# Kernel tuning notes

Hardware: AMD Instinct MI355X
Metric: run time of the kernel (lower is better)

The kernel has to match this reference:

```python
import jax, jax.numpy as jnp
import numpy as np

B, T, C, H = 4, 2048, 1024, 8
D = C // H


def _rope_tables(t, d, base=10000.0):
    inv = 1.0 / (base ** (jnp.arange(0, d, 2, dtype=jnp.float32) / d))
    freqs = jnp.outer(jnp.arange(t, dtype=jnp.float32), inv)  # (T, D/2)
    cos = jnp.concatenate([jnp.cos(freqs)] * 2, axis=-1)  # (T, D)
    sin = jnp.concatenate([jnp.sin(freqs)] * 2, axis=-1)
    return cos, sin


def _apply_rope(x, cos, sin):
    # x: (B,H,T,D); rotate-half RoPE
    d2 = x.shape[-1] // 2
    x1, x2 = x[..., :d2], x[..., d2:]
    rot = jnp.concatenate([-x2, x1], axis=-1)
    return x * cos + rot * sin


def setup_inputs() -> dict:
    key = jax.random.key(0)
    ks = jax.random.split(key, 8)
    x = jax.random.normal(ks[0], (B, T, C), jnp.float32)
    w = lambda k: jax.random.normal(k, (C, C), jnp.float32) * 0.02
    # trigram directions: 8 sign patterns in {-1,+1}^3, L2-normalized (as in get_trigrams + F.normalize)
    signs = np.array([[(1 if (i >> b) & 1 else -1) for b in range(3)] for i in range(8)], np.float32)
    head_dirs = jnp.asarray(signs / np.sqrt(3.0))
    return {
        'x': x,
        'Wq': w(ks[1]), 'Wk': w(ks[2]), 'Wv': w(ks[3]), 'Wo': w(ks[4]),
        'ln_g': jnp.ones((C,), jnp.float32), 'ln_b': jnp.zeros((C,), jnp.float32),
        'head_scales': jax.random.normal(ks[5], (H,), jnp.float32) * 0.1,
        'head_dirs': head_dirs,
    }


def reference(x, Wq, Wk, Wv, Wo, ln_g, ln_b, head_scales, head_dirs):
    b, t, c = x.shape
    h = head_dirs.shape[0]
    d = c // h
    scale = 1.0 / jnp.sqrt(jnp.asarray(d, x.dtype))
    # pre-LN
    mu = jnp.mean(x, axis=-1, keepdims=True)
    var = jnp.mean((x - mu) ** 2, axis=-1, keepdims=True)
    xn = (x - mu) * jax.lax.rsqrt(var + 1e-5) * ln_g + ln_b
    q = (xn @ Wq.T).reshape(b, t, h, d).transpose(0, 2, 1, 3)  # (B,H,T,D)
    k = (xn @ Wk.T).reshape(b, t, h, d).transpose(0, 2, 1, 3)
    v = (xn @ Wv.T).reshape(b, t, h, d).transpose(0, 2, 1, 3)
    cos, sin = _rope_tables(t, d)
    q = _apply_rope(q, cos, sin)
    k = _apply_rope(k, cos, sin)
    causal = jnp.tril(jnp.ones((t, t), bool))
    # standard causal SDPA
    scores = jnp.einsum('bhqd,bhkd->bhqk', q, k) * scale
    scores = jnp.where(causal, scores, -jnp.inf)
    attn = jax.nn.softmax(scores, axis=-1)
    out = jnp.einsum('bhqk,bhkd->bhqd', attn, v)
    # trigram geometric bias attention (rank-1 logits from first 3 dims)
    qp = jnp.einsum('bhtd,hd->bht', q[..., :3], head_dirs)
    kp = jnp.einsum('bhtd,hd->bht', k[..., :3], head_dirs)
    geo = qp[..., :, None] * kp[..., None, :]  # (B,H,T,T)
    geo = jnp.where(causal, geo, -jnp.inf)
    geo_attn = jax.nn.softmax(geo, axis=-1)
    geo_out = jnp.einsum('bhqk,bhkd->bhqd', geo_attn, v)
    out = out + head_scales[None, :, None, None] * jax.lax.stop_gradient(geo_out - out)
    out = out.transpose(0, 2, 1, 3).reshape(b, t, c) @ Wo.T
    return x + out
```

## Files before the change

### kernel.cpp

```cpp
#include <hip/hip_runtime.h>
#include <hip/hip_bf16.h>
#include <stdint.h>

#define BB 4
#define TT 2048
#define CC 1024
#define HH 8
#define DD 128

typedef unsigned short u16;
typedef unsigned int u32;
typedef unsigned long long u64;
typedef __attribute__((ext_vector_type(4))) float f32x4;
typedef __attribute__((ext_vector_type(16))) float f32x16;
typedef __attribute__((ext_vector_type(8))) __bf16 bf16x8;

__device__ __forceinline__ float bf2f(u16 u){ u32 x=((u32)u)<<16; float f; __builtin_memcpy(&f,&x,4); return f; }
__device__ __forceinline__ u16 f2bf(float f){ u32 x; __builtin_memcpy(&x,&f,4); x += 0x7fffu + ((x>>16)&1u); return (u16)(x>>16); }

__device__ __forceinline__ void gload16(const void* g, void* l){
  __builtin_amdgcn_global_load_lds((const __attribute__((address_space(1))) u32*)g,
                                   (__attribute__((address_space(3))) u32*)l, 16, 0, 0);
}
__device__ __forceinline__ f32x4 mfma16(bf16x8 a, bf16x8 b, f32x4 c){
  return __builtin_amdgcn_mfma_f32_16x16x32_bf16(a,b,c,0,0,0);
}
__device__ __forceinline__ f32x16 mfma32(bf16x8 a, bf16x8 b, f32x16 c){
  return __builtin_amdgcn_mfma_f32_32x32x16_bf16(a,b,c,0,0,0);
}
__device__ __forceinline__ u32 cvtpk(float lo, float hi){
  u32 r; asm("v_cvt_pk_bf16_f32 %0, %1, %2" : "=v"(r) : "v"(lo), "v"(hi)); return r;
}
__device__ __forceinline__ void pl32swap(u32& d, u32& s){
  asm volatile("v_permlane32_swap_b32 %0, %1" : "+v"(d), "+v"(s));
}
union FRAG { u32 u[4]; bf16x8 v; };

__global__ void ln_k(const float* __restrict__ x, const float* __restrict__ g,
                     const float* __restrict__ bta, u16* __restrict__ xn){
  int row = blockIdx.x, tid = threadIdx.x;
  const float4 v = ((const float4*)(x + (size_t)row*CC))[tid];
  float s = v.x+v.y+v.z+v.w;
  float ss = v.x*v.x+v.y*v.y+v.z*v.z+v.w*v.w;
  #pragma unroll
  for(int m=1;m<64;m<<=1){ s += __shfl_xor(s,m); ss += __shfl_xor(ss,m); }
  __shared__ float red[8];
  if((tid&63)==0){ red[tid>>6]=s; red[4+(tid>>6)]=ss; }
  __syncthreads();
  float ts = red[0]+red[1]+red[2]+red[3];
  float tss = red[4]+red[5]+red[6]+red[7];
  float mu = ts*(1.0f/CC);
  float rs = rsqrtf(tss*(1.0f/CC) - mu*mu + 1e-5f);
  int c0 = tid*4;
  ushort4 o;
  o.x = f2bf((v.x-mu)*rs*g[c0+0]+bta[c0+0]);
  o.y = f2bf((v.y-mu)*rs*g[c0+1]+bta[c0+1]);
  o.z = f2bf((v.z-mu)*rs*g[c0+2]+bta[c0+2]);
  o.w = f2bf((v.w-mu)*rs*g[c0+3]+bta[c0+3]);
  ((ushort4*)(xn + (size_t)row*CC))[tid] = o;
}

__global__ void wconv_k(const float* __restrict__ wq, const float* __restrict__ wk,
                        const float* __restrict__ wv, const float* __restrict__ wo,
                        u16* __restrict__ out){
  int i = blockIdx.x*256 + threadIdx.x;
  int sel = i>>18;
  const float* src = sel==0?wq: sel==1?wk: sel==2?wv:wo;
  float4 v = ((const float4*)src)[i & 262143];
  ushort4 o; o.x=f2bf(v.x); o.y=f2bf(v.y); o.z=f2bf(v.z); o.w=f2bf(v.w);
  ((ushort4*)out)[i] = o;
}

__global__ void rope_tab_k(float* __restrict__ cosT, float* __restrict__ sinT){
  int i = blockIdx.x*256 + threadIdx.x;
  int t = i>>6, j = i&63;
  float inv = powf(10000.0f, -(float)(2*j)*(1.0f/128.0f));
  float a = (float)t * inv;
  cosT[i] = cosf(a);
  sinT[i] = sinf(a);
}

__global__ void qpkp_k(const u16* __restrict__ Qb, const u16* __restrict__ Kb,
                       const float* __restrict__ dirs, const float* __restrict__ cosT,
                       const float* __restrict__ sinT, float* __restrict__ qp, float* __restrict__ kp){
  int idx = blockIdx.x*256 + threadIdx.x;
  int b = idx>>14, rem = idx & 16383;
  int h = rem>>11, t = rem & 2047;
  size_t base = ((size_t)(b*TT + t))*CC + h*DD;
  float qv = 0.f, kv = 0.f;
  #pragma unroll
  for(int d=0; d<3; d++){
    float c = cosT[t*64+d], s = sinT[t*64+d];
    float dr = dirs[h*3+d];
    qv += (bf2f(Qb[base+d])*c - bf2f(Qb[base+d+64])*s) * dr;
    kv += (bf2f(Kb[base+d])*c - bf2f(Kb[base+d+64])*s) * dr;
  }
  qp[idx] = qv; kp[idx] = kv;
}

__global__ void ropepack_k(u16* __restrict__ Qb, const u16* __restrict__ Kb,
                           u16* __restrict__ KF,
                           const float* __restrict__ cosT, const float* __restrict__ sinT){
  const float SL2 = 0.08838834764831845f * 1.442695040888963f;
  int bt = blockIdx.x, tid = threadIdx.x;
  int b = bt>>11, t = bt & (TT-1);
  int ks = t>>5, k31 = t&31;
  int p0 = tid*4;
  int h = p0>>6, d0 = p0&63;
  size_t i1 = (size_t)bt*CC + h*DD + d0;
  ushort4 q1v = *(const ushort4*)(Qb + i1);
  ushort4 q2v = *(const ushort4*)(Qb + i1 + 64);
  ushort4 k1v = *(const ushort4*)(Kb + i1);
  ushort4 k2v = *(const ushort4*)(Kb + i1 + 64);
  float4 cv = *(const float4*)(cosT + t*64 + d0);
  float4 sv = *(const float4*)(sinT + t*64 + d0);
  float q1[4] = {bf2f(q1v.x),bf2f(q1v.y),bf2f(q1v.z),bf2f(q1v.w)};
  float q2[4] = {bf2f(q2v.x),bf2f(q2v.y),bf2f(q2v.z),bf2f(q2v.w)};
  float k1[4] = {bf2f(k1v.x),bf2f(k1v.y),bf2f(k1v.z),bf2f(k1v.w)};
  float k2[4] = {bf2f(k2v.x),bf2f(k2v.y),bf2f(k2v.z),bf2f(k2v.w)};
  float cc[4] = {cv.x,cv.y,cv.z,cv.w};
  float ssn[4] = {sv.x,sv.y,sv.z,sv.w};
  ushort4 oq1, oq2, ok1, ok2;
  u16* oq1p = (u16*)&oq1; u16* oq2p = (u16*)&oq2;
  u16* ok1p = (u16*)&ok1; u16* ok2p = (u16*)&ok2;
  #pragma unroll
  for(int j=0;j<4;j++){
    oq1p[j] = f2bf((q1[j]*cc[j] - q2[j]*ssn[j])*SL2);
    oq2p[j] = f2bf((q2[j]*cc[j] + q1[j]*ssn[j])*SL2);
    ok1p[j] = f2bf(k1[j]*cc[j] - k2[j]*ssn[j]);
    ok2p[j] = f2bf(k2[j]*cc[j] + k1[j]*ssn[j]);
  }
  *(ushort4*)(Qb + i1)      = oq1;
  *(ushort4*)(Qb + i1 + 64) = oq2;
  int bh = b*HH + h;
  int d2 = d0 + 64;
  size_t o1 = (((size_t)(bh*64 + ks)*8) + (d0>>4))*512 + (((d0>>3)&1)*32 + k31)*8 + (d0&7);
  size_t o2 = (((size_t)(bh*64 + ks)*8) + (d2>>4))*512 + (((d2>>3)&1)*32 + k31)*8 + (d2&7);
  *(ushort4*)(KF + o1) = ok1;
  *(ushort4*)(KF + o2) = ok2;
}

template<int MODE>
__global__ __launch_bounds__(256) void gemm_k(const u16* __restrict__ A, const u16* __restrict__ W,
                                              u16* __restrict__ outb, float* __restrict__ outf,
                                              const float* __restrict__ resid){
  __shared__ __align__(16) u16 As[128*64];
  __shared__ __align__(16) u16 Bs[128*64];
  const int K = CC;
  int m0 = blockIdx.x*128, n0 = blockIdx.y*128;
  int tid = threadIdx.x, w = tid>>6, l = tid&63;
  int li = l&15, lg = l>>4;
  int wm = w>>1, wn = w&1;
  f32x4 acc[4][4] = {};
  for(int k0=0; k0<K; k0+=64){
    #pragma unroll
    for(int i=0;i<4;i++){
      int L = (w*4+i)*1024 + l*16;
      int row = L>>7;
      int colb = (L&127) ^ ((row&7)<<4);
      gload16(A + ((size_t)(m0+row)*K + k0 + (colb>>1)), (char*)As + (w*4+i)*1024);
      gload16(W + ((size_t)(n0+row)*K + k0 + (colb>>1)), (char*)Bs + (w*4+i)*1024);
    }
    __syncthreads();
    #pragma unroll
    for(int kc=0;kc<2;kc++){
      bf16x8 af[4], bfr[4];
      #pragma unroll
      for(int mi=0;mi<4;mi++){
        int row = wm*64 + mi*16 + li;
        int colb = (kc*64 + lg*16) ^ ((row&7)<<4);
        af[mi] = *(const bf16x8*)((const char*)As + row*128 + colb);
      }
      #pragma unroll
      for(int ni=0;ni<4;ni++){
        int row = wn*64 + ni*16 + li;
        int colb = (kc*64 + lg*16) ^ ((row&7)<<4);
        bfr[ni] = *(const bf16x8*)((const char*)Bs + row*128 + colb);
      }
      #pragma unroll
      for(int mi=0;mi<4;mi++){
        #pragma unroll
        for(int ni=0;ni<4;ni++)
          acc[mi][ni] = mfma16(af[mi], bfr[ni], acc[mi][ni]);
      }
    }
    __syncthreads();
  }
  #pragma unroll
  for(int mi=0;mi<4;mi++){
    #pragma unroll
    for(int ni=0;ni<4;ni++){
      if(MODE==4){
        int row0 = m0 + wm*64 + mi*16 + lg*4;
        int col = n0 + wn*64 + ni*16 + li;
        int t = row0 & 2047, b = row0>>11;
        int h = col>>7, d = col&127;
        int bh = b*HH + h;
        size_t o = (((size_t)(bh*64 + (t>>5))*8) + (d>>5)*2 + ((t>>4)&1))*512
                   + (((t>>3)&1)*32 + (d&31))*8 + (t&7);
        ushort4 pk;
        pk.x = f2bf(acc[mi][ni][0]); pk.y = f2bf(acc[mi][ni][1]);
        pk.z = f2bf(acc[mi][ni][2]); pk.w = f2bf(acc[mi][ni][3]);
        *(ushort4*)(outb + o) = pk;
      } else {
        #pragma unroll
        for(int r=0;r<4;r++){
          int row = m0 + wm*64 + mi*16 + lg*4 + r;
          int col = n0 + wn*64 + ni*16 + li;
          float v = acc[mi][ni][r];
          if(MODE==0){
            outb[(size_t)row*CC + col] = f2bf(v);
          } else {
            size_t o = (size_t)row*CC + col;
            outf[o] = v + resid[o];
          }
        }
      }
    }
  }
}

struct SegState { float m1, l1, m2, l2; f32x16 a1[4]; f32x16 a2[4]; };

__device__ __forceinline__ void run_seg(int t, int klo, int khi, int bh, int b, int h,
                                        int l5, int q31,
                                        const u16* __restrict__ Q, const u16* __restrict__ KF,
                                        const u16* __restrict__ VF, const float* __restrict__ qp,
                                        const float* __restrict__ kp, SegState& S){
  const f32x16 zf = {};
  S.m1 = -__builtin_inff(); S.l1 = 0.f; S.m2 = -__builtin_inff(); S.l2 = 0.f;
  #pragma unroll
  for(int dt=0;dt<4;dt++){ S.a1[dt] = zf; S.a2[dt] = zf; }
  if(khi <= klo) return;

  int q0 = t*32, q = q0 + q31;
  bf16x8 qf[8];
  {
    const u16* qbase = Q + ((size_t)(b*TT + q)*CC + h*DD);
    #pragma unroll
    for(int db=0;db<8;db++) qf[db] = *(const bf16x8*)(qbase + db*16 + l5*8);
  }
  const float L2E = 1.442695040888963f;
  bf16x8 qpf;
  {
    float qs = qp[(size_t)bh*TT + q] * L2E;
    u16 qh = f2bf(qs); float qhf = bf2f(qh);
    u16 ql = f2bf(qs - qhf);
    FRAG fq; fq.u[0] = l5? 0u : ((u32)qh | ((u32)qh<<16));
    fq.u[1] = l5? 0u : (u32)ql; fq.u[2]=0; fq.u[3]=0;
    qpf = fq.v;
  }
  const u16* kfp = KF + (size_t)bh*64*4096 + (size_t)klo*4096 + (size_t)(q31 + 32*l5)*8;
  const u16* vfp = VF + (size_t)bh*64*4096 + (size_t)klo*4096 + (size_t)(q31 + 32*l5)*8;
  const float* kpp = kp + (size_t)bh*TT + q31;

  for(int is=klo; is<khi; ++is){
    int ksub = is*32;

    bf16x8 kf0 = *(const bf16x8*)(kfp + 0*512);
    bf16x8 kf1 = *(const bf16x8*)(kfp + 1*512);
    bf16x8 kf2 = *(const bf16x8*)(kfp + 2*512);
    bf16x8 kf3 = *(const bf16x8*)(kfp + 3*512);
    bf16x8 kf4 = *(const bf16x8*)(kfp + 4*512);
    bf16x8 kf5 = *(const bf16x8*)(kfp + 5*512);
    bf16x8 kf6 = *(const bf16x8*)(kfp + 6*512);
    bf16x8 kf7 = *(const bf16x8*)(kfp + 7*512);

    f32x16 s0 = {}, s1a = {};
    __builtin_amdgcn_s_setprio(1);
    s0  = mfma32(kf0, qf[0], s0);  s1a = mfma32(kf1, qf[1], s1a);
    s0  = mfma32(kf2, qf[2], s0);  s1a = mfma32(kf3, qf[3], s1a);
    s0  = mfma32(kf4, qf[4], s0);  s1a = mfma32(kf5, qf[5], s1a);
    s0  = mfma32(kf6, qf[6], s0);  s1a = mfma32(kf7, qf[7], s1a);
    __builtin_amdgcn_s_setprio(0);

    f32x16 gg;
    {
      const f32x16 zf2 = {};
      float kpv = kpp[ksub];
      u16 kh = f2bf(kpv); float khf = bf2f(kh);
      u16 kl = f2bf(kpv - khf);
      FRAG fk; fk.u[0] = l5? 0u : ((u32)kh | ((u32)kl<<16));
      fk.u[1] = l5? 0u : (u32)kh; fk.u[2]=0; fk.u[3]=0;
      gg = mfma32(fk.v, qpf, zf2);
    }

    float sv[16], gv[16];
    #pragma unroll
    for(int rr=0;rr<16;rr++){ sv[rr] = s0[rr]+s1a[rr]; gv[rr] = gg[rr]; }
    if(ksub + 31 > q0){
      #pragma unroll
      for(int rr=0;rr<16;rr++){
        int kg = ksub + (rr&3) + 8*(rr>>2) + 4*l5;
        if(kg > q){ sv[rr] = -__builtin_inff(); gv[rr] = -__builtin_inff(); }
      }
    }

    float mx=-__builtin_inff(), gx=-__builtin_inff();
    #pragma unroll
    for(int rr=0;rr<16;rr++){ mx = fmaxf(mx, sv[rr]); gx = fmaxf(gx, gv[rr]); }
    mx = fmaxf(mx, __shfl_xor(mx,32));
    gx = fmaxf(gx, __shfl_xor(gx,32));
    if(__ballot((mx > S.m1+8.f) | (gx > S.m2+8.f))){
      float mn1 = fmaxf(S.m1,mx), mn2 = fmaxf(S.m2,gx);
      float c1 = exp2f(S.m1-mn1), c2 = exp2f(S.m2-mn2);
      S.l1 *= c1; S.l2 *= c2; S.m1 = mn1; S.m2 = mn2;
      #pragma unroll
      for(int dt=0;dt<4;dt++){ S.a1[dt] *= c1; S.a2[dt] *= c2; }
    }
    float rs1=0.f, rs2=0.f;
    float e1[16], e2[16];
    #pragma unroll
    for(int rr=0;rr<16;rr++){
      e1[rr] = exp2f(sv[rr] - S.m1); rs1 += e1[rr];
      e2[rr] = exp2f(gv[rr] - S.m2); rs2 += e2[rr];
    }
    rs1 += __shfl_xor(rs1,32); rs2 += __shfl_xor(rs2,32);
    S.l1 += rs1; S.l2 += rs2;

    u32 P1[8], P2[8];
    #pragma unroll
    for(int m=0;m<8;m++){ P1[m] = cvtpk(e1[2*m], e1[2*m+1]); P2[m] = cvtpk(e2[2*m], e2[2*m+1]); }
    pl32swap(P1[0],P1[2]); pl32swap(P1[1],P1[3]); pl32swap(P1[4],P1[6]); pl32swap(P1[5],P1[7]);
    pl32swap(P2[0],P2[2]); pl32swap(P2[1],P2[3]); pl32swap(P2[4],P2[6]); pl32swap(P2[5],P2[7]);

    #pragma unroll
    for(int kb2=0;kb2<2;kb2++){
      FRAG f1, f2;
      #pragma unroll
      for(int j2=0;j2<4;j2++){ f1.u[j2] = P1[kb2*4+j2]; f2.u[j2] = P2[kb2*4+j2]; }
      bf16x8 pb1 = f1.v, pb2 = f2.v;
      bf16x8 vf0 = *(const bf16x8*)(vfp + (0+kb2)*512);
      bf16x8 vf1 = *(const bf16x8*)(vfp + (2+kb2)*512);
      bf16x8 vf2 = *(const bf16x8*)(vfp + (4+kb2)*512);
      bf16x8 vf3 = *(const bf16x8*)(vfp + (6+kb2)*512);
      __builtin_amdgcn_s_setprio(1);
      S.a1[0] = mfma32(vf0, pb1, S.a1[0]);  S.a2[0] = mfma32(vf0, pb2, S.a2[0]);
      S.a1[1] = mfma32(vf1, pb1, S.a1[1]);  S.a2[1] = mfma32(vf1, pb2, S.a2[1]);
      S.a1[2] = mfma32(vf2, pb1, S.a1[2]);  S.a2[2] = mfma32(vf2, pb2, S.a2[2]);
      S.a1[3] = mfma32(vf3, pb1, S.a1[3]);  S.a2[3] = mfma32(vf3, pb2, S.a2[3]);
      __builtin_amdgcn_s_setprio(0);
    }
    kfp += 4096; vfp += 4096;
  }
}

__global__ __launch_bounds__(128,2) void attn_k(const u16* __restrict__ Q, const u16* __restrict__ KF,
                                                const u16* __restrict__ VF, const float* __restrict__ qp,
                                                const float* __restrict__ kp, const float* __restrict__ hs,
                                                u16* __restrict__ outp){
  __shared__ __align__(16) float lp1[4*64*16];
  __shared__ __align__(16) float lp2[4*64*16];
  __shared__ float lml[32*4];
  int bid = blockIdx.x;
  int xcd = bid&7, r = bid>>3;
  int bh = xcd*4 + (r&3);
  int p = r>>2;
  int b = bh>>3, h = bh&7;
  int tid = threadIdx.x, w = tid>>6, l = tid&63;
  int l5 = l>>5, q31 = l&31;
  float sh = hs[h];

  SegState S;
  if(w==0){
    run_seg(p, 0, p+1, bh, b, h, l5, q31, Q, KF, VF, qp, kp, S);
    {
      float rl1 = 1.0f/S.l1, rl2 = 1.0f/S.l2;
      int q = p*32 + q31;
      u16* obase = outp + (size_t)(b*TT + q)*CC + h*DD;
      #pragma unroll
      for(int dt=0;dt<4;dt++){
        #pragma unroll
        for(int m=0;m<8;m++){
          float oa1 = S.a1[dt][2*m]*rl1,   oa2 = S.a2[dt][2*m]*rl2;
          float ob1 = S.a1[dt][2*m+1]*rl1, ob2 = S.a2[dt][2*m+1]*rl2;
          float oa = oa1 + sh*(oa2-oa1);
          float ob = ob1 + sh*(ob2-ob1);
          int d = dt*32 + (2*m&3) + 8*(m>>1) + 4*l5;
          *(u32*)(obase + d) = cvtpk(oa, ob);
        }
      }
    }
    run_seg(63-p, 0, 31-p, bh, b, h, l5, q31, Q, KF, VF, qp, kp, S);
    #pragma unroll
    for(int dt=0;dt<4;dt++){
      *(f32x16*)&lp1[(dt*64 + l)*16] = S.a1[dt];
      *(f32x16*)&lp2[(dt*64 + l)*16] = S.a2[dt];
    }
    if(l5==0){
      lml[q31*4+0] = S.m1; lml[q31*4+1] = S.l1;
      lml[q31*4+2] = S.m2; lml[q31*4+3] = S.l2;
    }
    __syncthreads();
  } else {
    run_seg(63-p, 31-p, 64-p, bh, b, h, l5, q31, Q, KF, VF, qp, kp, S);
    __syncthreads();
    float mA1 = lml[q31*4+0], lA1 = lml[q31*4+1];
    float mA2 = lml[q31*4+2], lA2 = lml[q31*4+3];
    float M1 = fmaxf(mA1, S.m1), M2 = fmaxf(mA2, S.m2);
    float wA1 = exp2f(mA1-M1), wB1 = exp2f(S.m1-M1);
    float wA2 = exp2f(mA2-M2), wB2 = exp2f(S.m2-M2);
    float r1 = 1.0f/(wA1*lA1 + wB1*S.l1);
    float r2 = 1.0f/(wA2*lA2 + wB2*S.l2);
    int q = (63-p)*32 + q31;
    u16* obase = outp + (size_t)(b*TT + q)*CC + h*DD;
    #pragma unroll
    for(int dt=0;dt<4;dt++){
      f32x16 pa1 = *(const f32x16*)&lp1[(dt*64 + l)*16];
      f32x16 pa2 = *(const f32x16*)&lp2[(dt*64 + l)*16];
      #pragma unroll
      for(int m=0;m<8;m++){
        float oa1 = (wA1*pa1[2*m]   + wB1*S.a1[dt][2*m])*r1;
        float ob1 = (wA1*pa1[2*m+1] + wB1*S.a1[dt][2*m+1])*r1;
        float oa2 = (wA2*pa2[2*m]   + wB2*S.a2[dt][2*m])*r2;
        float ob2 = (wA2*pa2[2*m+1] + wB2*S.a2[dt][2*m+1])*r2;
        float oa = oa1 + sh*(oa2-oa1);
        float ob = ob1 + sh*(ob2-ob1);
        int d = dt*32 + (2*m&3) + 8*(m>>1) + 4*l5;
        *(u32*)(obase + d) = cvtpk(oa, ob);
      }
    }
  }
}

extern "C" void kernel_launch(void* const* d_in, const int* in_sizes, int n_in,
                              void* d_out, int out_size, void* d_ws, size_t ws_size,
                              hipStream_t stream){
  (void)in_sizes; (void)n_in; (void)out_size; (void)ws_size;
  const float* x   = (const float*)d_in[0];
  const float* Wq  = (const float*)d_in[1];
  const float* Wk  = (const float*)d_in[2];
  const float* Wv  = (const float*)d_in[3];
  const float* Wo  = (const float*)d_in[4];
  const float* lng = (const float*)d_in[5];
  const float* lnb = (const float*)d_in[6];
  const float* hsc = (const float*)d_in[7];
  const float* hdr = (const float*)d_in[8];

  char* ws = (char*)d_ws;
  const size_t MB = 1048576;
  u16* xn   = (u16*)ws;
  u16* wbf  = (u16*)(ws + 16*MB);
  u16* Qb   = (u16*)(ws + 24*MB);
  u16* Kb   = (u16*)(ws + 40*MB);
  u16* VF   = (u16*)(ws + 56*MB);
  u16* KF   = (u16*)(ws + 72*MB);
  float* cosT = (float*)(ws + 88*MB);
  float* sinT = cosT + 131072;
  float* qp   = sinT + 131072;
  float* kp   = qp + 65536;

  ln_k<<<8192,256,0,stream>>>(x, lng, lnb, xn);
  wconv_k<<<4096,256,0,stream>>>(Wq,Wk,Wv,Wo,wbf);
  rope_tab_k<<<512,256,0,stream>>>(cosT,sinT);
  gemm_k<0><<<dim3(64,8),256,0,stream>>>(xn, wbf,          Qb, nullptr, nullptr);
  gemm_k<0><<<dim3(64,8),256,0,stream>>>(xn, wbf+1048576,  Kb, nullptr, nullptr);
  gemm_k<4><<<dim3(64,8),256,0,stream>>>(xn, wbf+2097152,  VF, nullptr, nullptr);
  qpkp_k<<<256,256,0,stream>>>(Qb,Kb,hdr,cosT,sinT,qp,kp);
  ropepack_k<<<8192,128,0,stream>>>(Qb,Kb,KF,cosT,sinT);
  attn_k<<<1024,128,0,stream>>>(Qb,KF,VF,qp,kp,hsc,xn);
  gemm_k<2><<<dim3(64,8),256,0,stream>>>(xn, wbf+3145728, nullptr, (float*)d_out, x);
}
```

Before: 230.3 us.

## Fuse RoPE and K repacking into QKV GEMM epilogue; merge prep kernels

The Q and K projection GEMMs now stage their output tile in shared memory and apply RoPE in the epilogue. Q is written pre-scaled and K goes straight into the attention fragment layout, so the separate ropepack kernel and the Kb intermediate buffer are removed. Weight conversion and RoPE table generation are merged into one launch. qp/kp are now derived from the already-rotated Q and K, with the softmax scale undone on the Q side. This saves a full read and write of Q and K plus two launches. In exchange the GEMM epilogue gets an extra LDS round trip and a sync, and qp/kp now come from bf16-rounded rotated values.

```diff
diff --git a/kernel.cpp b/kernel.cpp
--- a/kernel.cpp
+++ b/kernel.cpp
@@ -14,6 +14,8 @@
 typedef __attribute__((ext_vector_type(4))) float f32x4;
 typedef __attribute__((ext_vector_type(16))) float f32x16;
 typedef __attribute__((ext_vector_type(8))) __bf16 bf16x8;
+
+#define SL2C (0.08838834764831845f * 1.442695040888963f)
 
 __device__ __forceinline__ float bf2f(u16 u){ u32 x=((u32)u)<<16; float f; __builtin_memcpy(&f,&x,4); return f; }
 __device__ __forceinline__ u16 f2bf(float f){ u32 x; __builtin_memcpy(&x,&f,4); x += 0x7fffu + ((x>>16)&1u); return (u16)(x>>16); }
@@ -60,92 +62,48 @@
   ((ushort4*)(xn + (size_t)row*CC))[tid] = o;
 }
 
-__global__ void wconv_k(const float* __restrict__ wq, const float* __restrict__ wk,
-                        const float* __restrict__ wv, const float* __restrict__ wo,
-                        u16* __restrict__ out){
-  int i = blockIdx.x*256 + threadIdx.x;
-  int sel = i>>18;
-  const float* src = sel==0?wq: sel==1?wk: sel==2?wv:wo;
-  float4 v = ((const float4*)src)[i & 262143];
-  ushort4 o; o.x=f2bf(v.x); o.y=f2bf(v.y); o.z=f2bf(v.z); o.w=f2bf(v.w);
-  ((ushort4*)out)[i] = o;
-}
-
-__global__ void rope_tab_k(float* __restrict__ cosT, float* __restrict__ sinT){
-  int i = blockIdx.x*256 + threadIdx.x;
-  int t = i>>6, j = i&63;
-  float inv = powf(10000.0f, -(float)(2*j)*(1.0f/128.0f));
-  float a = (float)t * inv;
-  cosT[i] = cosf(a);
-  sinT[i] = sinf(a);
-}
-
-__global__ void qpkp_k(const u16* __restrict__ Qb, const u16* __restrict__ Kb,
-                       const float* __restrict__ dirs, const float* __restrict__ cosT,
-                       const float* __restrict__ sinT, float* __restrict__ qp, float* __restrict__ kp){
+__global__ void prep_k(const float* __restrict__ wq, const float* __restrict__ wk,
+                       const float* __restrict__ wv, const float* __restrict__ wo,
+                       u16* __restrict__ out, float* __restrict__ cosT, float* __restrict__ sinT){
+  if(blockIdx.x < 4096){
+    int i = blockIdx.x*256 + threadIdx.x;
+    int sel = i>>18;
+    const float* src = sel==0?wq: sel==1?wk: sel==2?wv:wo;
+    float4 v = ((const float4*)src)[i & 262143];
+    ushort4 o; o.x=f2bf(v.x); o.y=f2bf(v.y); o.z=f2bf(v.z); o.w=f2bf(v.w);
+    ((ushort4*)out)[i] = o;
+  } else {
+    int i = (blockIdx.x-4096)*256 + threadIdx.x;
+    int t = i>>6, j = i&63;
+    float inv = powf(10000.0f, -(float)(2*j)*(1.0f/128.0f));
+    float a = (float)t * inv;
+    cosT[i] = cosf(a);
+    sinT[i] = sinf(a);
+  }
+}
+
+__global__ void qpkp_k(const u16* __restrict__ Qb, const u16* __restrict__ KF,
+                       const float* __restrict__ dirs, float* __restrict__ qp, float* __restrict__ kp){
+  const float INV_SL2 = 1.0f/SL2C;
   int idx = blockIdx.x*256 + threadIdx.x;
   int b = idx>>14, rem = idx & 16383;
   int h = rem>>11, t = rem & 2047;
-  size_t base = ((size_t)(b*TT + t))*CC + h*DD;
-  float qv = 0.f, kv = 0.f;
-  #pragma unroll
-  for(int d=0; d<3; d++){
-    float c = cosT[t*64+d], s = sinT[t*64+d];
-    float dr = dirs[h*3+d];
-    qv += (bf2f(Qb[base+d])*c - bf2f(Qb[base+d+64])*s) * dr;
-    kv += (bf2f(Kb[base+d])*c - bf2f(Kb[base+d+64])*s) * dr;
-  }
-  qp[idx] = qv; kp[idx] = kv;
-}
-
-__global__ void ropepack_k(u16* __restrict__ Qb, const u16* __restrict__ Kb,
-                           u16* __restrict__ KF,
-                           const float* __restrict__ cosT, const float* __restrict__ sinT){
-  const float SL2 = 0.08838834764831845f * 1.442695040888963f;
-  int bt = blockIdx.x, tid = threadIdx.x;
-  int b = bt>>11, t = bt & (TT-1);
-  int ks = t>>5, k31 = t&31;
-  int p0 = tid*4;
-  int h = p0>>6, d0 = p0&63;
-  size_t i1 = (size_t)bt*CC + h*DD + d0;
-  ushort4 q1v = *(const ushort4*)(Qb + i1);
-  ushort4 q2v = *(const ushort4*)(Qb + i1 + 64);
-  ushort4 k1v = *(const ushort4*)(Kb + i1);
-  ushort4 k2v = *(const ushort4*)(Kb + i1 + 64);
-  float4 cv = *(const float4*)(cosT + t*64 + d0);
-  float4 sv = *(const float4*)(sinT + t*64 + d0);
-  float q1[4] = {bf2f(q1v.x),bf2f(q1v.y),bf2f(q1v.z),bf2f(q1v.w)};
-  float q2[4] = {bf2f(q2v.x),bf2f(q2v.y),bf2f(q2v.z),bf2f(q2v.w)};
-  float k1[4] = {bf2f(k1v.x),bf2f(k1v.y),bf2f(k1v.z),bf2f(k1v.w)};
-  float k2[4] = {bf2f(k2v.x),bf2f(k2v.y),bf2f(k2v.z),bf2f(k2v.w)};
-  float cc[4] = {cv.x,cv.y,cv.z,cv.w};
-  float ssn[4] = {sv.x,sv.y,sv.z,sv.w};
-  ushort4 oq1, oq2, ok1, ok2;
-  u16* oq1p = (u16*)&oq1; u16* oq2p = (u16*)&oq2;
-  u16* ok1p = (u16*)&ok1; u16* ok2p = (u16*)&ok2;
-  #pragma unroll
-  for(int j=0;j<4;j++){
-    oq1p[j] = f2bf((q1[j]*cc[j] - q2[j]*ssn[j])*SL2);
-    oq2p[j] = f2bf((q2[j]*cc[j] + q1[j]*ssn[j])*SL2);
-    ok1p[j] = f2bf(k1[j]*cc[j] - k2[j]*ssn[j]);
-    ok2p[j] = f2bf(k2[j]*cc[j] + k1[j]*ssn[j]);
-  }
-  *(ushort4*)(Qb + i1)      = oq1;
-  *(ushort4*)(Qb + i1 + 64) = oq2;
   int bh = b*HH + h;
-  int d2 = d0 + 64;
-  size_t o1 = (((size_t)(bh*64 + ks)*8) + (d0>>4))*512 + (((d0>>3)&1)*32 + k31)*8 + (d0&7);
-  size_t o2 = (((size_t)(bh*64 + ks)*8) + (d2>>4))*512 + (((d2>>3)&1)*32 + k31)*8 + (d2&7);
-  *(ushort4*)(KF + o1) = ok1;
-  *(ushort4*)(KF + o2) = ok2;
+  float d0 = dirs[h*3], d1 = dirs[h*3+1], d2 = dirs[h*3+2];
+  size_t qbase = ((size_t)(b*TT + t))*CC + h*DD;
+  qp[idx] = (bf2f(Qb[qbase])*d0 + bf2f(Qb[qbase+1])*d1 + bf2f(Qb[qbase+2])*d2) * INV_SL2;
+  size_t kb = ((size_t)(bh*64 + (t>>5))*8)*512 + (size_t)(t&31)*8;
+  kp[idx] = bf2f(KF[kb])*d0 + bf2f(KF[kb+1])*d1 + bf2f(KF[kb+2])*d2;
 }
 
 template<int MODE>
 __global__ __launch_bounds__(256) void gemm_k(const u16* __restrict__ A, const u16* __restrict__ W,
                                               u16* __restrict__ outb, float* __restrict__ outf,
-                                              const float* __restrict__ resid){
-  __shared__ __align__(16) u16 As[128*64];
-  __shared__ __align__(16) u16 Bs[128*64];
+                                              const float* __restrict__ resid,
+                                              const float* __restrict__ cosT, const float* __restrict__ sinT){
+  __shared__ __align__(16) u16 sbuf[16384];
+  u16* As = sbuf;
+  u16* Bs = sbuf + 8192;
   const int K = CC;
   int m0 = blockIdx.x*128, n0 = blockIdx.y*128;
   int tid = threadIdx.x, w = tid>>6, l = tid&63;
@@ -186,6 +144,60 @@
     }
     __syncthreads();
   }
+
+  if(MODE==0 || MODE==5){
+    #pragma unroll
+    for(int mi=0;mi<4;mi++){
+      #pragma unroll
+      for(int ni=0;ni<4;ni++){
+        int c = wn*64 + ni*16 + li;
+        #pragma unroll
+        for(int r=0;r<4;r++){
+          int rr = wm*64 + mi*16 + lg*4 + r;
+          sbuf[rr*128 + (c ^ ((rr&15)<<3))] = f2bf(acc[mi][ni][r]);
+        }
+      }
+    }
+    __syncthreads();
+    int rowl = tid & 127, half = tid >> 7;
+    int grow = m0 + rowl;
+    int t = grow & (TT-1);
+    int swz = (rowl&15)<<3;
+    const float* cbase = cosT + t*64;
+    const float* sbase = sinT + t*64;
+    #pragma unroll
+    for(int g=0; g<16; g++){
+      int c0 = half*64 + g*4;
+      int j0 = c0 & 63;
+      float4 cv = *(const float4*)(cbase + j0);
+      float4 sv4 = *(const float4*)(sbase + j0);
+      ushort4 se4 = *(const ushort4*)&sbuf[rowl*128 + (c0 ^ swz)];
+      ushort4 pa4 = *(const ushort4*)&sbuf[rowl*128 + ((c0^64) ^ swz)];
+      float se[4] = {bf2f(se4.x),bf2f(se4.y),bf2f(se4.z),bf2f(se4.w)};
+      float pa[4] = {bf2f(pa4.x),bf2f(pa4.y),bf2f(pa4.z),bf2f(pa4.w)};
+      float cc4[4] = {cv.x,cv.y,cv.z,cv.w};
+      float ss4[4] = {sv4.x,sv4.y,sv4.z,sv4.w};
+      ushort4 o; u16* op = (u16*)&o;
+      #pragma unroll
+      for(int e=0;e<4;e++){
+        float v = half ? (se[e]*cc4[e] + pa[e]*ss4[e]) : (se[e]*cc4[e] - pa[e]*ss4[e]);
+        if(MODE==0) v *= SL2C;
+        op[e] = f2bf(v);
+      }
+      if(MODE==0){
+        *(ushort4*)(outb + (size_t)grow*CC + n0 + c0) = o;
+      } else {
+        int b = grow>>11;
+        int h = n0>>7;
+        int bh = b*HH + h;
+        int d0 = c0;
+        size_t of = (((size_t)(bh*64 + (t>>5))*8) + (d0>>4))*512 + (((d0>>3)&1)*32 + (t&31))*8 + (d0&7);
+        *(ushort4*)(outb + of) = o;
+      }
+    }
+    return;
+  }
+
   #pragma unroll
   for(int mi=0;mi<4;mi++){
     #pragma unroll
@@ -207,13 +219,8 @@
         for(int r=0;r<4;r++){
           int row = m0 + wm*64 + mi*16 + lg*4 + r;
           int col = n0 + wn*64 + ni*16 + li;
-          float v = acc[mi][ni][r];
-          if(MODE==0){
-            outb[(size_t)row*CC + col] = f2bf(v);
-          } else {
-            size_t o = (size_t)row*CC + col;
-            outf[o] = v + resid[o];
-          }
+          size_t o = (size_t)row*CC + col;
+          outf[o] = acc[mi][ni][r] + resid[o];
         }
       }
     }
@@ -442,7 +449,6 @@
   u16* xn   = (u16*)ws;
   u16* wbf  = (u16*)(ws + 16*MB);
   u16* Qb   = (u16*)(ws + 24*MB);
-  u16* Kb   = (u16*)(ws + 40*MB);
   u16* VF   = (u16*)(ws + 56*MB);
   u16* KF   = (u16*)(ws + 72*MB);
   float* cosT = (float*)(ws + 88*MB);
@@ -451,13 +457,11 @@
   float* kp   = qp + 65536;
 
   ln_k<<<8192,256,0,stream>>>(x, lng, lnb, xn);
-  wconv_k<<<4096,256,0,stream>>>(Wq,Wk,Wv,Wo,wbf);
-  rope_tab_k<<<512,256,0,stream>>>(cosT,sinT);
-  gemm_k<0><<<dim3(64,8),256,0,stream>>>(xn, wbf,          Qb, nullptr, nullptr);
-  gemm_k<0><<<dim3(64,8),256,0,stream>>>(xn, wbf+1048576,  Kb, nullptr, nullptr);
-  gemm_k<4><<<dim3(64,8),256,0,stream>>>(xn, wbf+2097152,  VF, nullptr, nullptr);
-  qpkp_k<<<256,256,0,stream>>>(Qb,Kb,hdr,cosT,sinT,qp,kp);
-  ropepack_k<<<8192,128,0,stream>>>(Qb,Kb,KF,cosT,sinT);
+  prep_k<<<4608,256,0,stream>>>(Wq,Wk,Wv,Wo,wbf,cosT,sinT);
+  gemm_k<0><<<dim3(64,8),256,0,stream>>>(xn, wbf,          Qb, nullptr, nullptr, cosT, sinT);
+  gemm_k<5><<<dim3(64,8),256,0,stream>>>(xn, wbf+1048576,  KF, nullptr, nullptr, cosT, sinT);
+  gemm_k<4><<<dim3(64,8),256,0,stream>>>(xn, wbf+2097152,  VF, nullptr, nullptr, nullptr, nullptr);
+  qpkp_k<<<256,256,0,stream>>>(Qb,KF,hdr,qp,kp);
   attn_k<<<1024,128,0,stream>>>(Qb,KF,VF,qp,kp,hsc,xn);
-  gemm_k<2><<<dim3(64,8),256,0,stream>>>(xn, wbf+3145728, nullptr, (float*)d_out, x);
-}
+  gemm_k<2><<<dim3(64,8),256,0,stream>>>(xn, wbf+3145728, nullptr, (float*)d_out, x, nullptr, nullptr);
+}
```

Measured after the change: 225.3 us (median of 2 runs). 1.02x faster.
